# Performance work log

Measured on AMD Instinct MI355X. Metric: run time of the kernel, lower is better.

## Reference

```python
import jax, jax.numpy as jnp
import numpy as np

B, S, D, H = 32, 512, 256, 4
DK = D // H  # d_k = d_q = d_v = 64


def setup_inputs() -> dict:
    key = jax.random.key(0)
    ks = jax.random.split(key, 10)
    lim_qk = np.sqrt(6.0 / (D + DK))  # xavier_uniform for [DK, D] linears
    lim_h = np.sqrt(6.0 / (DK + D))
    return {
        "q": jax.random.normal(ks[0], (B, S, D), jnp.float32),
        "k": jax.random.normal(ks[1], (B, S, D), jnp.float32),
        "v": jax.random.normal(ks[2], (B, S, D), jnp.float32),
        # causal mask: True where attention is disallowed (masked_fill -inf)
        "mask": jnp.triu(jnp.ones((1, S, S), bool), k=1),
        # per-head query/key projections, stacked over heads: [H, DK, D]
        "Wq": jax.random.uniform(ks[3], (H, DK, D), jnp.float32, -lim_qk, lim_qk),
        "bq": jnp.zeros((H, DK), jnp.float32),
        "Wk": jax.random.uniform(ks[4], (H, DK, D), jnp.float32, -lim_qk, lim_qk),
        "bk": jnp.zeros((H, DK), jnp.float32),
        # shared value projection: [DK, D]
        "Wv": jax.random.uniform(ks[5], (DK, D), jnp.float32, -lim_qk, lim_qk),
        "bv": jnp.zeros((DK,), jnp.float32),
        # output head projection (no bias): [D, DK]
        "Wh": jax.random.uniform(ks[6], (D, DK), jnp.float32, -lim_h, lim_h),
    }


def reference(q, k, v, mask, Wq, bq, Wk, bk, Wv, bv, Wh):
    # shared V projection: [B, S, DK]
    vs = jnp.einsum("bsd,kd->bsk", v, Wv) + bv
    # per-head Q/K projections, batched over heads: [B, H, S, DK]
    qs = jnp.einsum("bsd,hkd->bhsk", q, Wq) + bq[None, :, None, :]
    ksp = jnp.einsum("bsd,hkd->bhsk", k, Wk) + bk[None, :, None, :]
    scale = jnp.sqrt(jnp.asarray(DK, jnp.float32))
    scores = jnp.einsum("bhsk,bhtk->bhst", qs, ksp) / scale  # [B, H, S, S]
    scores = jnp.where(mask[:, None, :, :], -jnp.inf, scores)
    attn = jax.nn.softmax(scores, axis=-1)  # [B, H, S, S]
    heads = jnp.einsum("bhst,btk->bhsk", attn, vs)  # [B, H, S, DK]
    out = jnp.mean(heads, axis=1)  # mean over heads -> [B, S, DK]
    out = jnp.einsum("bsk,dk->bsd", out, Wh)  # [B, S, D]
    # torch stacks attns at dim=2 -> [B, S, H, S]
    return out, jnp.transpose(attn, (0, 2, 1, 3))
```

## Files before the change

### kernel.cpp

```cpp
#include <hip/hip_runtime.h>
#include <math.h>

#define B_  32
#define S_  512
#define D_  256
#define H_  4
#define DK_ 64

typedef float  f32x4 __attribute__((ext_vector_type(4)));
typedef short  s16x8 __attribute__((ext_vector_type(8)));
typedef unsigned short u16x4 __attribute__((ext_vector_type(4)));
typedef unsigned int   u32x4 __attribute__((ext_vector_type(4)));

#define MFMA_BF16(a, b, c) __builtin_amdgcn_mfma_f32_16x16x32_bf16((a), (b), (c), 0, 0, 0)
#define GLOAD_LDS16(g, l)                                                      \
  __builtin_amdgcn_global_load_lds(                                            \
      (const __attribute__((address_space(1))) void*)(g),                      \
      (__attribute__((address_space(3))) void*)(l), 16, 0, 0)

#if __has_builtin(__builtin_amdgcn_exp2f)
#define EXP2(x) __builtin_amdgcn_exp2f(x)
#else
#define EXP2(x) __expf((x) * 0.6931471805599453f)
#endif

#define QSCALE 0.18033688011112042f

__device__ __forceinline__ unsigned short f2bf(float x) {
  unsigned int u = __float_as_uint(x);
  unsigned int r = (u + 0x7FFFu + ((u >> 16) & 1u)) >> 16;
  return (unsigned short)r;
}

__device__ __forceinline__ float bf2f(unsigned short u) {
  return __uint_as_float((unsigned int)u << 16);
}

__device__ __forceinline__ unsigned cvtpk(float lo, float hi) {
  unsigned r;
  asm("v_cvt_pk_bf16_f32 %0, %1, %2" : "=v"(r) : "v"(lo), "v"(hi));
  return r;
}

__device__ __forceinline__ s16x8 cvt8(const float* p) {
  float4 a = *(const float4*)p;
  float4 b = *(const float4*)(p + 4);
  s16x8 r;
  r[0] = (short)f2bf(a.x); r[1] = (short)f2bf(a.y);
  r[2] = (short)f2bf(a.z); r[3] = (short)f2bf(a.w);
  r[4] = (short)f2bf(b.x); r[5] = (short)f2bf(b.y);
  r[6] = (short)f2bf(b.z); r[7] = (short)f2bf(b.w);
  return r;
}

__global__ void wconv_kernel(const float* __restrict__ Wq, const float* __restrict__ Wk,
                             const float* __restrict__ Wv, const float* __restrict__ Wh,
                             unsigned short* __restrict__ out) {
  int i = blockIdx.x * 256 + threadIdx.x;
  float v, sc = 1.f;
  if (i < 65536)        { v = Wq[i];          sc = QSCALE; }
  else if (i < 131072)  { v = Wk[i - 65536]; }
  else if (i < 147456)  { v = Wv[i - 131072]; }
  else                  { v = Wh[i - 147456]; sc = 0.25f; }
  out[i] = f2bf(v * sc);
}

__global__ __launch_bounds__(256) void proj_kernel(
    const float* __restrict__ q, const float* __restrict__ k, const float* __restrict__ v,
    const unsigned short* __restrict__ Wb,
    const float* __restrict__ bq, const float* __restrict__ bk, const float* __restrict__ bv,
    unsigned short* __restrict__ qs, unsigned short* __restrict__ ks,
    unsigned short* __restrict__ vst) {
  const int y = blockIdx.y;
  const int m0 = blockIdx.x * 64;
  const int b = m0 >> 9, s0 = m0 & (S_ - 1);
  const int tid = threadIdx.x, w = tid >> 6, l = tid & 63;
  const int lr = l & 15, lg = l >> 4;
  const float* src = (y == 0) ? q : (y == 1) ? k : v;
  const float* abase = src + (size_t)(m0 + w * 16 + lr) * D_;

  __shared__ __align__(16) unsigned short Wsl[16384];

  const int nrows = (y < 2) ? 256 : 64;
  const unsigned short* wbase = Wb + (size_t)(y * 256) * D_;

  auto stW = [&](int k0) {
    const int nbytes = nrows * 128;
    for (int p = tid * 16; p < nbytes; p += 4096) {
      int row = p >> 7, c = (p >> 4) & 7;
      GLOAD_LDS16((const char*)(wbase + (size_t)row * D_ + k0) + ((c ^ (row & 7)) << 4),
                  (char*)Wsl + p);
    }
  };
  auto WF = [&](int row, int c) -> s16x8 {
    return *(const s16x8*)((const char*)Wsl + row * 128 + ((c ^ (row & 7)) << 4));
  };

  if (y < 2) {
    f32x4 acc[4][4] = {};
    for (int k0 = 0; k0 < D_; k0 += 64) {
      stW(k0);
      s16x8 af0 = cvt8(abase + k0 + 8 * lg);
      s16x8 af1 = cvt8(abase + k0 + 32 + 8 * lg);
      __syncthreads();
#pragma unroll
      for (int h = 0; h < 4; ++h) {
#pragma unroll
        for (int ns = 0; ns < 4; ++ns) {
          s16x8 wf0 = WF(h * 64 + ns * 16 + lr, lg);
          s16x8 wf1 = WF(h * 64 + ns * 16 + lr, 4 + lg);
          acc[h][ns] = MFMA_BF16(af0, wf0, acc[h][ns]);
          acc[h][ns] = MFMA_BF16(af1, wf1, acc[h][ns]);
        }
      }
      __syncthreads();
    }
    const float* bias = (y == 0) ? bq : bk;
    const float bsc = (y == 0) ? QSCALE : 1.f;
    unsigned short* dst = (y == 0) ? qs : ks;
#pragma unroll
    for (int h = 0; h < 4; ++h) {
#pragma unroll
      for (int ns = 0; ns < 4; ++ns) {
        int dk = ns * 16 + lr;
        float bb = bias[h * 64 + dk] * bsc;
#pragma unroll
        for (int i = 0; i < 4; ++i) {
          int s = s0 + w * 16 + lg * 4 + i;
          dst[(((size_t)b * H_ + h) * S_ + s) * DK_ + dk] = f2bf(acc[h][ns][i] + bb);
        }
      }
    }
  } else {
    f32x4 acc[4] = {};
    for (int k0 = 0; k0 < D_; k0 += 64) {
      stW(k0);
      s16x8 af0 = cvt8(abase + k0 + 8 * lg);
      s16x8 af1 = cvt8(abase + k0 + 32 + 8 * lg);
      __syncthreads();
#pragma unroll
      for (int ns = 0; ns < 4; ++ns) {
        s16x8 wf0 = WF(ns * 16 + lr, lg);
        s16x8 wf1 = WF(ns * 16 + lr, 4 + lg);
        acc[ns] = MFMA_BF16(af0, wf0, acc[ns]);
        acc[ns] = MFMA_BF16(af1, wf1, acc[ns]);
      }
      __syncthreads();
    }
#pragma unroll
    for (int ns = 0; ns < 4; ++ns) {
      int dk = ns * 16 + lr;
      float bb = bv[dk];
      u16x4 pk;
#pragma unroll
      for (int i = 0; i < 4; ++i) pk[i] = f2bf(acc[ns][i] + bb);
      int t = s0 + w * 16 + lg * 4;
      *(u16x4*)(vst + ((size_t)b * DK_ + dk) * S_ + t) = pk;
    }
  }
}

__global__ __launch_bounds__(512) void attn_kernel(
    const unsigned short* __restrict__ qs, const unsigned short* __restrict__ ks,
    const unsigned short* __restrict__ vst, float* __restrict__ attn,
    unsigned short* __restrict__ hh) {
  const int m = blockIdx.x;
  const int half = m >> 8, g = (m >> 1) & 1;
  const int stp = half ? (3 - g) : g;
  const int rem = ((m >> 2) & 63) * 2 + (m & 1);
  const int b = rem & 31, h = rem >> 5;
  const int tid = threadIdx.x, w = tid >> 6, l = tid & 63;
  const int lr = l & 15, lg = l >> 4;
  const int S0 = stp * 128;
  const int dtile = 2 * stp + (w >> 2);
  const int NT = 2 * stp + 2;

  __shared__ __align__(16) unsigned short Kb[2][4096];
  __shared__ __align__(16) unsigned short Vb[2][4096];
  __shared__ __align__(16) unsigned short Pb[8][16][72];

  const unsigned short* qb = qs + ((size_t)b * H_ + h) * S_ * DK_;
  const char* kbase = (const char*)(ks + ((size_t)b * H_ + h) * S_ * DK_);
  const char* vbase = (const char*)(vst + (size_t)b * DK_ * S_);

  auto stK = [&](int buf, int t0) {
    int p = tid * 16;
    int row = p >> 7, c = (p >> 4) & 7;
    GLOAD_LDS16(kbase + (size_t)t0 * 128 + row * 128 + ((c ^ (row & 7)) << 4),
                (char*)&Kb[buf][0] + p);
  };
  auto stV = [&](int buf, int t0) {
    int p = tid * 16;
    int row = p >> 7, c = (p >> 4) & 7;
    GLOAD_LDS16(vbase + (size_t)row * 1024 + t0 * 2 + ((c ^ (row & 7)) << 4),
                (char*)&Vb[buf][0] + p);
  };
  auto KF = [&](int buf, int row, int c) -> s16x8 {
    return *(const s16x8*)((const char*)&Kb[buf][0] + row * 128 + ((c ^ (row & 7)) << 4));
  };
  auto VF = [&](int buf, int row, int c) -> s16x8 {
    return *(const s16x8*)((const char*)&Vb[buf][0] + row * 128 + ((c ^ (row & 7)) << 4));
  };

  s16x8 qf0 = *(const s16x8*)(qb + (size_t)(S0 + w * 16 + lr) * DK_ + 8 * lg);
  s16x8 qf1 = *(const s16x8*)(qb + (size_t)(S0 + w * 16 + lr) * DK_ + 32 + 8 * lg);

  float lsum[4] = {0.f, 0.f, 0.f, 0.f};

  stK(0, 0);
  __syncthreads();
  for (int tt = 0; tt < NT; ++tt) {
    const int cur = tt & 1;
    if (tt + 1 < NT) stK(cur ^ 1, tt * 64 + 64);
    if (tt <= dtile) {
#pragma unroll
      for (int ts = 0; ts < 4; ++ts) {
        s16x8 kf0 = KF(cur, ts * 16 + lr, lg);
        s16x8 kf1 = KF(cur, ts * 16 + lr, 4 + lg);
        f32x4 acc = {};
        acc = MFMA_BF16(qf0, kf0, acc);
        acc = MFMA_BF16(qf1, kf1, acc);
        if (tt == dtile) {
          int tg = tt * 64 + ts * 16 + lr;
#pragma unroll
          for (int i = 0; i < 4; ++i) {
            int sg = S0 + w * 16 + lg * 4 + i;
            lsum[i] += EXP2((tg > sg) ? -1e30f : acc[i]);
          }
        } else {
#pragma unroll
          for (int i = 0; i < 4; ++i) lsum[i] += EXP2(acc[i]);
        }
      }
    }
    __syncthreads();
  }
#pragma unroll
  for (int off = 1; off < 16; off <<= 1) {
#pragma unroll
    for (int i = 0; i < 4; ++i) lsum[i] += __shfl_xor(lsum[i], off);
  }
  float lg2s[4];
#pragma unroll
  for (int i = 0; i < 4; ++i) lg2s[i] = __log2f(lsum[i]);

  stK(0, 0);
  stV(0, 0);
  __syncthreads();
  f32x4 oacc[4] = {};
  for (int tt = 0; tt < NT; ++tt) {
    const int t0 = tt * 64;
    const int cur = tt & 1;
    if (tt + 1 < NT) { stK(cur ^ 1, t0 + 64); stV(cur ^ 1, t0 + 64); }
    if (tt <= dtile) {
#pragma unroll
      for (int ts = 0; ts < 4; ++ts) {
        s16x8 kf0 = KF(cur, ts * 16 + lr, lg);
        s16x8 kf1 = KF(cur, ts * 16 + lr, 4 + lg);
        f32x4 acc = {};
        acc = MFMA_BF16(qf0, kf0, acc);
        acc = MFMA_BF16(qf1, kf1, acc);
        int tg = t0 + ts * 16 + lr;
        float p[4];
        if (tt == dtile) {
#pragma unroll
          for (int i = 0; i < 4; ++i) {
            int sg = S0 + w * 16 + lg * 4 + i;
            p[i] = EXP2(((tg > sg) ? -1e30f : acc[i]) - lg2s[i]);
          }
        } else {
#pragma unroll
          for (int i = 0; i < 4; ++i) p[i] = EXP2(acc[i] - lg2s[i]);
        }
#pragma unroll
        for (int i = 0; i < 4; ++i) {
          int sg = S0 + w * 16 + lg * 4 + i;
          attn[(((size_t)b * S_ + sg) * H_ + h) * S_ + tg] = p[i];
        }
        unsigned pk0 = cvtpk(p[0], p[1]);
        unsigned pk1 = cvtpk(p[2], p[3]);
        Pb[w][lg * 4 + 0][ts * 16 + lr] = (unsigned short)pk0;
        Pb[w][lg * 4 + 1][ts * 16 + lr] = (unsigned short)(pk0 >> 16);
        Pb[w][lg * 4 + 2][ts * 16 + lr] = (unsigned short)pk1;
        Pb[w][lg * 4 + 3][ts * 16 + lr] = (unsigned short)(pk1 >> 16);
      }
      asm volatile("s_waitcnt lgkmcnt(0)" ::: "memory");
      __builtin_amdgcn_sched_barrier(0);
      s16x8 pa0 = *(const s16x8*)(&Pb[w][lr][8 * lg]);
      s16x8 pa1 = *(const s16x8*)(&Pb[w][lr][32 + 8 * lg]);
#pragma unroll
      for (int ds = 0; ds < 4; ++ds) {
        s16x8 vf0 = VF(cur, ds * 16 + lr, lg);
        s16x8 vf1 = VF(cur, ds * 16 + lr, 4 + lg);
        oacc[ds] = MFMA_BF16(pa0, vf0, oacc[ds]);
        oacc[ds] = MFMA_BF16(pa1, vf1, oacc[ds]);
      }
    }
    __syncthreads();
  }

  for (int tt = dtile + 1; tt < 8; ++tt) {
    const int t0 = tt * 64;
    f32x4 z = {};
#pragma unroll
    for (int i = 0; i < 4; ++i) {
      int sg = S0 + w * 16 + lg * 4 + i;
      *(f32x4*)(attn + (((size_t)b * S_ + sg) * H_ + h) * S_ + t0 + lr * 4) = z;
    }
  }

#pragma unroll
  for (int ds = 0; ds < 4; ++ds) {
#pragma unroll
    for (int i = 0; i < 4; ++i) {
      int s = S0 + w * 16 + lg * 4 + i;
      hh[(((size_t)b * H_ + h) * S_ + s) * DK_ + ds * 16 + lr] = f2bf(oacc[ds][i]);
    }
  }
}

__global__ __launch_bounds__(256) void houtproj_kernel(
    const unsigned short* __restrict__ hh, const unsigned short* __restrict__ Whb,
    float* __restrict__ out) {
  const int m0 = blockIdx.x * 64, n0 = blockIdx.y * 64;
  const int tid = threadIdx.x, w = tid >> 6, l = tid & 63;
  const int lr = l & 15, lg = l >> 4;
  const int row = m0 + w * 16 + lr;
  const int b = row >> 9, s = row & (S_ - 1);

  __shared__ __align__(16) unsigned short Whs[4096];

#pragma unroll
  for (int it = 0; it < 2; ++it) {
    int p = it * 4096 + tid * 16;
    int r = p >> 7, c = (p >> 4) & 7;
    GLOAD_LDS16((const char*)(Whb + (size_t)(n0 + r) * DK_) + ((c ^ (r & 7)) << 4),
                (char*)Whs + p);
  }

  s16x8 af[2];
#pragma unroll
  for (int kk = 0; kk < 2; ++kk) {
    float sum8[8] = {};
#pragma unroll
    for (int hd = 0; hd < 4; ++hd) {
      s16x8 x = *(const s16x8*)(hh + (((size_t)b * H_ + hd) * S_ + s) * DK_ + kk * 32 + 8 * lg);
#pragma unroll
      for (int e = 0; e < 8; ++e) sum8[e] += bf2f((unsigned short)x[e]);
    }
    u32x4 pk;
#pragma unroll
    for (int j = 0; j < 4; ++j) pk[j] = cvtpk(sum8[2 * j], sum8[2 * j + 1]);
    af[kk] = *(s16x8*)&pk;
  }
  __syncthreads();

  auto WHF = [&](int r, int c) -> s16x8 {
    return *(const s16x8*)((const char*)Whs + r * 128 + ((c ^ (r & 7)) << 4));
  };
  f32x4 acc[4] = {};
#pragma unroll
  for (int ns = 0; ns < 4; ++ns) {
    s16x8 wf0 = WHF(ns * 16 + lr, lg);
    s16x8 wf1 = WHF(ns * 16 + lr, 4 + lg);
    acc[ns] = MFMA_BF16(af[0], wf0, acc[ns]);
    acc[ns] = MFMA_BF16(af[1], wf1, acc[ns]);
  }
#pragma unroll
  for (int ns = 0; ns < 4; ++ns) {
#pragma unroll
    for (int i = 0; i < 4; ++i) {
      out[(size_t)(m0 + w * 16 + lg * 4 + i) * D_ + n0 + ns * 16 + lr] = acc[ns][i];
    }
  }
}

extern "C" void kernel_launch(void* const* d_in, const int* in_sizes, int n_in,
                              void* d_out, int out_size, void* d_ws, size_t ws_size,
                              hipStream_t stream) {
  (void)in_sizes; (void)n_in; (void)out_size; (void)ws_size;
  const float* q  = (const float*)d_in[0];
  const float* k  = (const float*)d_in[1];
  const float* v  = (const float*)d_in[2];
  const float* Wq = (const float*)d_in[4];
  const float* bq = (const float*)d_in[5];
  const float* Wk = (const float*)d_in[6];
  const float* bk = (const float*)d_in[7];
  const float* Wv = (const float*)d_in[8];
  const float* bv = (const float*)d_in[9];
  const float* Wh = (const float*)d_in[10];

  float* out  = (float*)d_out;
  float* attn = out + (size_t)B_ * S_ * D_;

  char* ws = (char*)d_ws;
  unsigned short* Wb  = (unsigned short*)ws;
  unsigned short* qs  = (unsigned short*)(ws + 327680);
  unsigned short* ksp = (unsigned short*)(ws + 327680 + 8388608);
  unsigned short* vst = (unsigned short*)(ws + 327680 + 16777216);
  unsigned short* hh  = (unsigned short*)(ws + 327680 + 18874368);

  wconv_kernel<<<640, 256, 0, stream>>>(Wq, Wk, Wv, Wh, Wb);
  proj_kernel<<<dim3(256, 3), 256, 0, stream>>>(q, k, v, Wb, bq, bk, bv, qs, ksp, vst);
  attn_kernel<<<512, 512, 0, stream>>>(qs, ksp, vst, attn, hh);
  houtproj_kernel<<<dim3(256, 4), 256, 0, stream>>>(hh, Wb + 147456, out);
}
```

Before: 62.62 us.

## Load K and V fragments directly from global memory instead of LDS staging

Removes the double-buffered LDS staging of K and V tiles (global_load_lds plus block-wide barriers) and has each wave read its MFMA fragments straight from global memory. Each wave now loops only up to its own diagonal tile, with no __syncthreads between tiles, so waves in a block no longer wait on each other. The cost is redundant global/L2 traffic, since all 8 waves re-read the same K/V rows, and no explicit prefetch overlap.

```diff
diff --git a/kernel.cpp b/kernel.cpp
--- a/kernel.cpp
+++ b/kernel.cpp
@@ -173,130 +173,97 @@
   const int lr = l & 15, lg = l >> 4;
   const int S0 = stp * 128;
   const int dtile = 2 * stp + (w >> 2);
-  const int NT = 2 * stp + 2;
-
-  __shared__ __align__(16) unsigned short Kb[2][4096];
-  __shared__ __align__(16) unsigned short Vb[2][4096];
+
   __shared__ __align__(16) unsigned short Pb[8][16][72];
 
   const unsigned short* qb = qs + ((size_t)b * H_ + h) * S_ * DK_;
-  const char* kbase = (const char*)(ks + ((size_t)b * H_ + h) * S_ * DK_);
-  const char* vbase = (const char*)(vst + (size_t)b * DK_ * S_);
-
-  auto stK = [&](int buf, int t0) {
-    int p = tid * 16;
-    int row = p >> 7, c = (p >> 4) & 7;
-    GLOAD_LDS16(kbase + (size_t)t0 * 128 + row * 128 + ((c ^ (row & 7)) << 4),
-                (char*)&Kb[buf][0] + p);
-  };
-  auto stV = [&](int buf, int t0) {
-    int p = tid * 16;
-    int row = p >> 7, c = (p >> 4) & 7;
-    GLOAD_LDS16(vbase + (size_t)row * 1024 + t0 * 2 + ((c ^ (row & 7)) << 4),
-                (char*)&Vb[buf][0] + p);
-  };
-  auto KF = [&](int buf, int row, int c) -> s16x8 {
-    return *(const s16x8*)((const char*)&Kb[buf][0] + row * 128 + ((c ^ (row & 7)) << 4));
-  };
-  auto VF = [&](int buf, int row, int c) -> s16x8 {
-    return *(const s16x8*)((const char*)&Vb[buf][0] + row * 128 + ((c ^ (row & 7)) << 4));
-  };
+  const unsigned short* kb = ks + ((size_t)b * H_ + h) * S_ * DK_;
+  const unsigned short* vb = vst + (size_t)b * DK_ * S_;
 
   s16x8 qf0 = *(const s16x8*)(qb + (size_t)(S0 + w * 16 + lr) * DK_ + 8 * lg);
   s16x8 qf1 = *(const s16x8*)(qb + (size_t)(S0 + w * 16 + lr) * DK_ + 32 + 8 * lg);
 
   float lsum[4] = {0.f, 0.f, 0.f, 0.f};
 
-  stK(0, 0);
-  __syncthreads();
-  for (int tt = 0; tt < NT; ++tt) {
-    const int cur = tt & 1;
-    if (tt + 1 < NT) stK(cur ^ 1, tt * 64 + 64);
-    if (tt <= dtile) {
-#pragma unroll
-      for (int ts = 0; ts < 4; ++ts) {
-        s16x8 kf0 = KF(cur, ts * 16 + lr, lg);
-        s16x8 kf1 = KF(cur, ts * 16 + lr, 4 + lg);
-        f32x4 acc = {};
-        acc = MFMA_BF16(qf0, kf0, acc);
-        acc = MFMA_BF16(qf1, kf1, acc);
-        if (tt == dtile) {
-          int tg = tt * 64 + ts * 16 + lr;
-#pragma unroll
-          for (int i = 0; i < 4; ++i) {
-            int sg = S0 + w * 16 + lg * 4 + i;
-            lsum[i] += EXP2((tg > sg) ? -1e30f : acc[i]);
-          }
-        } else {
-#pragma unroll
-          for (int i = 0; i < 4; ++i) lsum[i] += EXP2(acc[i]);
-        }
-      }
-    }
-    __syncthreads();
-  }
-#pragma unroll
-  for (int off = 1; off < 16; off <<= 1) {
-#pragma unroll
-    for (int i = 0; i < 4; ++i) lsum[i] += __shfl_xor(lsum[i], off);
-  }
-  float lg2s[4];
-#pragma unroll
-  for (int i = 0; i < 4; ++i) lg2s[i] = __log2f(lsum[i]);
-
-  stK(0, 0);
-  stV(0, 0);
-  __syncthreads();
-  f32x4 oacc[4] = {};
-  for (int tt = 0; tt < NT; ++tt) {
+  for (int tt = 0; tt <= dtile; ++tt) {
     const int t0 = tt * 64;
-    const int cur = tt & 1;
-    if (tt + 1 < NT) { stK(cur ^ 1, t0 + 64); stV(cur ^ 1, t0 + 64); }
-    if (tt <= dtile) {
-#pragma unroll
-      for (int ts = 0; ts < 4; ++ts) {
-        s16x8 kf0 = KF(cur, ts * 16 + lr, lg);
-        s16x8 kf1 = KF(cur, ts * 16 + lr, 4 + lg);
-        f32x4 acc = {};
-        acc = MFMA_BF16(qf0, kf0, acc);
-        acc = MFMA_BF16(qf1, kf1, acc);
+#pragma unroll
+    for (int ts = 0; ts < 4; ++ts) {
+      const unsigned short* kr = kb + (size_t)(t0 + ts * 16 + lr) * DK_;
+      s16x8 kf0 = *(const s16x8*)(kr + 8 * lg);
+      s16x8 kf1 = *(const s16x8*)(kr + 32 + 8 * lg);
+      f32x4 acc = {};
+      acc = MFMA_BF16(qf0, kf0, acc);
+      acc = MFMA_BF16(qf1, kf1, acc);
+      if (tt == dtile) {
         int tg = t0 + ts * 16 + lr;
-        float p[4];
-        if (tt == dtile) {
-#pragma unroll
-          for (int i = 0; i < 4; ++i) {
-            int sg = S0 + w * 16 + lg * 4 + i;
-            p[i] = EXP2(((tg > sg) ? -1e30f : acc[i]) - lg2s[i]);
-          }
-        } else {
-#pragma unroll
-          for (int i = 0; i < 4; ++i) p[i] = EXP2(acc[i] - lg2s[i]);
-        }
 #pragma unroll
         for (int i = 0; i < 4; ++i) {
           int sg = S0 + w * 16 + lg * 4 + i;
-          attn[(((size_t)b * S_ + sg) * H_ + h) * S_ + tg] = p[i];
+          lsum[i] += EXP2((tg > sg) ? -1e30f : acc[i]);
         }
-        unsigned pk0 = cvtpk(p[0], p[1]);
-        unsigned pk1 = cvtpk(p[2], p[3]);
-        Pb[w][lg * 4 + 0][ts * 16 + lr] = (unsigned short)pk0;
-        Pb[w][lg * 4 + 1][ts * 16 + lr] = (unsigned short)(pk0 >> 16);
-        Pb[w][lg * 4 + 2][ts * 16 + lr] = (unsigned short)pk1;
-        Pb[w][lg * 4 + 3][ts * 16 + lr] = (unsigned short)(pk1 >> 16);
-      }
-      asm volatile("s_waitcnt lgkmcnt(0)" ::: "memory");
-      __builtin_amdgcn_sched_barrier(0);
-      s16x8 pa0 = *(const s16x8*)(&Pb[w][lr][8 * lg]);
-      s16x8 pa1 = *(const s16x8*)(&Pb[w][lr][32 + 8 * lg]);
-#pragma unroll
-      for (int ds = 0; ds < 4; ++ds) {
-        s16x8 vf0 = VF(cur, ds * 16 + lr, lg);
-        s16x8 vf1 = VF(cur, ds * 16 + lr, 4 + lg);
-        oacc[ds] = MFMA_BF16(pa0, vf0, oacc[ds]);
-        oacc[ds] = MFMA_BF16(pa1, vf1, oacc[ds]);
-      }
-    }
-    __syncthreads();
+      } else {
+#pragma unroll
+        for (int i = 0; i < 4; ++i) lsum[i] += EXP2(acc[i]);
+      }
+    }
+  }
+#pragma unroll
+  for (int off = 1; off < 16; off <<= 1) {
+#pragma unroll
+    for (int i = 0; i < 4; ++i) lsum[i] += __shfl_xor(lsum[i], off);
+  }
+  float lg2s[4];
+#pragma unroll
+  for (int i = 0; i < 4; ++i) lg2s[i] = __log2f(lsum[i]);
+
+  f32x4 oacc[4] = {};
+  for (int tt = 0; tt <= dtile; ++tt) {
+    const int t0 = tt * 64;
+#pragma unroll
+    for (int ts = 0; ts < 4; ++ts) {
+      const unsigned short* kr = kb + (size_t)(t0 + ts * 16 + lr) * DK_;
+      s16x8 kf0 = *(const s16x8*)(kr + 8 * lg);
+      s16x8 kf1 = *(const s16x8*)(kr + 32 + 8 * lg);
+      f32x4 acc = {};
+      acc = MFMA_BF16(qf0, kf0, acc);
+      acc = MFMA_BF16(qf1, kf1, acc);
+      int tg = t0 + ts * 16 + lr;
+      float p[4];
+      if (tt == dtile) {
+#pragma unroll
+        for (int i = 0; i < 4; ++i) {
+          int sg = S0 + w * 16 + lg * 4 + i;
+          p[i] = EXP2(((tg > sg) ? -1e30f : acc[i]) - lg2s[i]);
+        }
+      } else {
+#pragma unroll
+        for (int i = 0; i < 4; ++i) p[i] = EXP2(acc[i] - lg2s[i]);
+      }
+#pragma unroll
+      for (int i = 0; i < 4; ++i) {
+        int sg = S0 + w * 16 + lg * 4 + i;
+        attn[(((size_t)b * S_ + sg) * H_ + h) * S_ + tg] = p[i];
+      }
+      unsigned pk0 = cvtpk(p[0], p[1]);
+      unsigned pk1 = cvtpk(p[2], p[3]);
+      Pb[w][lg * 4 + 0][ts * 16 + lr] = (unsigned short)pk0;
+      Pb[w][lg * 4 + 1][ts * 16 + lr] = (unsigned short)(pk0 >> 16);
+      Pb[w][lg * 4 + 2][ts * 16 + lr] = (unsigned short)pk1;
+      Pb[w][lg * 4 + 3][ts * 16 + lr] = (unsigned short)(pk1 >> 16);
+    }
+    asm volatile("s_waitcnt lgkmcnt(0)" ::: "memory");
+    __builtin_amdgcn_sched_barrier(0);
+    s16x8 pa0 = *(const s16x8*)(&Pb[w][lr][8 * lg]);
+    s16x8 pa1 = *(const s16x8*)(&Pb[w][lr][32 + 8 * lg]);
+#pragma unroll
+    for (int ds = 0; ds < 4; ++ds) {
+      const unsigned short* vr = vb + (size_t)(ds * 16 + lr) * S_ + t0;
+      s16x8 vf0 = *(const s16x8*)(vr + 8 * lg);
+      s16x8 vf1 = *(const s16x8*)(vr + 32 + 8 * lg);
+      oacc[ds] = MFMA_BF16(pa0, vf0, oacc[ds]);
+      oacc[ds] = MFMA_BF16(pa1, vf1, oacc[ds]);
+    }
   }
 
   for (int tt = dtile + 1; tt < 8; ++tt) {
```

Result: slower. 93.17 us (+48.8%).
